# Optimization experiments

Measured on AMD Instinct MI355X. Metric: run time of the kernel, lower is better.

Reference implementation:

```python
import jax, jax.numpy as jnp
import numpy as np

D, E, H, K = 1024, 8, 4096, 2
B, S = 4, 2048


def setup_inputs() -> dict:
    key = jax.random.key(0)
    ks = jax.random.split(key, 5)
    scale = 0.02
    return {
        "x": jax.random.normal(ks[0], (B, S, D), dtype=jnp.float32),
        "gate_w": jax.random.normal(ks[1], (D, E), dtype=jnp.float32) * scale,
        "w1": jax.random.normal(ks[2], (E, D, H), dtype=jnp.float32) * scale,
        "b1": jnp.zeros((E, H), dtype=jnp.float32),
        "w2": jax.random.normal(ks[3], (E, H, D), dtype=jnp.float32) * scale,
        "b2": jnp.zeros((E, D), dtype=jnp.float32),
        "top_k": K,
    }


def reference(x, gate_w, w1, b1, w2, b2, top_k):
    orig_shape = x.shape
    d = x.shape[-1]
    xt = x.reshape(-1, d)                      # [T, D]
    T = xt.shape[0]

    # Gating: top-k over expert scores, softmax over the selected k.
    scores = xt @ gate_w                       # [T, E]
    expert_weights, expert_indices = jax.lax.top_k(scores, top_k)  # [T, K]
    expert_weights = jax.nn.softmax(expert_weights, axis=-1)

    # Dense all-expert MLP (GPT-style fc -> GELU -> proj), batched over experts.
    h = jnp.einsum('td,edh->eth', xt, w1) + b1[:, None, :]   # [E, T, H]
    h = jax.nn.gelu(h, approximate=False)
    outs = jnp.einsum('eth,ehd->etd', h, w2) + b2[:, None, :]  # [E, T, D]

    # Combine: gather each token's selected experts and mix with gate weights.
    tok = jnp.arange(T)[:, None]               # [T, 1]
    gathered = outs[expert_indices, tok]       # [T, K, D]
    y = jnp.sum(gathered * expert_weights[..., None], axis=1)  # [T, D]
    return y.reshape(orig_shape)
```

## Files before the change

### kernel.cpp

```cpp
#include <hip/hip_runtime.h>
#include <stdint.h>

#define T_TOK 8192
#define D_DIM 1024
#define E_NUM 8
#define H_DIM 4096

#define BM 128
#define BN 128
#define BK 64
#define NSEG 8
#define MAX_ROWS2 17408
#define MAX_MT2 (MAX_ROWS2/BM)

typedef unsigned short u16;
typedef __attribute__((ext_vector_type(8))) short shortx8;
typedef __attribute__((ext_vector_type(4))) float floatx4;
typedef __attribute__((ext_vector_type(8))) unsigned short ushortx8;

typedef const __attribute__((address_space(1))) unsigned int g_uint;
typedef __attribute__((address_space(3))) unsigned int l_uint;

__device__ __forceinline__ u16 f2bf(float f) {
  union { float f; unsigned int u; } v; v.f = f;
  unsigned int r = v.u + 0x7FFFu + ((v.u >> 16) & 1u);
  return (u16)(r >> 16);
}
__device__ __forceinline__ void gld_lds16(const u16* g, u16* l) {
  __builtin_amdgcn_global_load_lds((g_uint*)g, (l_uint*)l, 16, 0, 0);
}
__device__ __forceinline__ float gelu_fast(float v) {
  float y = v * (1.5957691216f + 0.07135481627f * v * v);
  y = fminf(y, 30.f);
  float ey = __expf(y);
  return v * ey * __builtin_amdgcn_rcpf(1.f + ey);
}

__global__ __launch_bounds__(256) void init_kernel(int* counts, int* fills, int* row_token) {
  int i = blockIdx.x * 256 + threadIdx.x;
  if (i < MAX_ROWS2) row_token[i] = -1;
  if (blockIdx.x == 0 && threadIdx.x < NSEG) { counts[threadIdx.x] = 0; fills[threadIdx.x] = 0; }
}

__global__ __launch_bounds__(256) void zero4_kernel(float4* out) {
  out[(size_t)blockIdx.x * 256 + threadIdx.x] = float4{0.f, 0.f, 0.f, 0.f};
}

__global__ __launch_bounds__(256) void convert_x_kernel(const float* __restrict__ X, u16* __restrict__ XC) {
  size_t i = ((size_t)blockIdx.x * 256 + threadIdx.x) * 8;
  float4 a = *(const float4*)&X[i];
  float4 b = *(const float4*)&X[i + 4];
  ushortx8 o;
  o[0] = f2bf(a.x); o[1] = f2bf(a.y); o[2] = f2bf(a.z); o[3] = f2bf(a.w);
  o[4] = f2bf(b.x); o[5] = f2bf(b.y); o[6] = f2bf(b.z); o[7] = f2bf(b.w);
  *(ushortx8*)&XC[i] = o;
}

__global__ __launch_bounds__(256) void gate_kernel(const float* __restrict__ X, const float* __restrict__ GW,
                                                   int* __restrict__ tk_idx, float* __restrict__ tk_w,
                                                   int* __restrict__ counts) {
  const int lane = threadIdx.x & 63;
  const int t = blockIdx.x * 4 + (threadIdx.x >> 6);
  const float4* xr4 = (const float4*)(X + (size_t)t * D_DIM + lane * 16);
  const float4* gw4 = (const float4*)GW;
  float acc[E_NUM];
#pragma unroll
  for (int e = 0; e < E_NUM; e++) acc[e] = 0.f;
#pragma unroll
  for (int i4 = 0; i4 < 4; i4++) {
    float4 xv = xr4[i4];
#pragma unroll
    for (int c = 0; c < 4; c++) {
      float xs = (&xv.x)[c];
      int d = lane * 16 + i4 * 4 + c;
      float4 g0 = gw4[d * 2], g1 = gw4[d * 2 + 1];
      acc[0] += xs * g0.x; acc[1] += xs * g0.y; acc[2] += xs * g0.z; acc[3] += xs * g0.w;
      acc[4] += xs * g1.x; acc[5] += xs * g1.y; acc[6] += xs * g1.z; acc[7] += xs * g1.w;
    }
  }
#pragma unroll
  for (int e = 0; e < E_NUM; e++)
    for (int off = 32; off; off >>= 1) acc[e] += __shfl_xor(acc[e], off);
  if (lane == 0) {
    int i0 = 0; float v0 = acc[0];
#pragma unroll
    for (int e = 1; e < E_NUM; e++) if (acc[e] > v0) { v0 = acc[e]; i0 = e; }
    int i1 = -1; float v1 = -1e30f;
#pragma unroll
    for (int e = 0; e < E_NUM; e++) if (e != i0 && acc[e] > v1) { v1 = acc[e]; i1 = e; }
    float e1 = expf(v1 - v0);
    float inv = 1.f / (1.f + e1);
    tk_idx[t * 2] = i0; tk_idx[t * 2 + 1] = i1;
    tk_w[t * 2] = inv;  tk_w[t * 2 + 1] = e1 * inv;
    atomicAdd(&counts[i0], 1); atomicAdd(&counts[i1], 1);
  }
}

__global__ void prefix_kernel(const int* counts, int* seg) {
  if (threadIdx.x == 0 && blockIdx.x == 0) {
    int a = 0;
    for (int i = 0; i < NSEG; i++) { seg[i] = a; a += ((counts[i] + BM - 1) / BM) * BM; }
    seg[NSEG] = a;
  }
}

__global__ __launch_bounds__(256) void fill_kernel(const int* __restrict__ tk_idx, const float* __restrict__ tk_w,
                                                   const int* __restrict__ seg, int* __restrict__ fills,
                                                   int* __restrict__ row_token, float* __restrict__ row_weight,
                                                   int* __restrict__ row_of) {
  int t = blockIdx.x * 256 + threadIdx.x;
  if (t >= T_TOK) return;
#pragma unroll
  for (int s = 0; s < 2; s++) {
    int sidx = tk_idx[t * 2 + s];
    int pos = atomicAdd(&fills[sidx], 1);
    int r = seg[sidx] + pos;
    row_token[r] = t; row_weight[r] = tk_w[t * 2 + s];
    row_of[t * 2 + s] = r;
  }
}

__global__ __launch_bounds__(256) void transpose_kernel(const float* __restrict__ src, u16* __restrict__ dst,
                                                        int R, int C) {
  __shared__ u16 tile[64][68];
  const int tid = threadIdx.x;
  size_t off = (size_t)blockIdx.z * (size_t)R * C;
  int r0 = blockIdx.y * 64, c0 = blockIdx.x * 64;
  int rr = tid >> 4, cc = (tid & 15) * 4;
#pragma unroll
  for (int i = 0; i < 4; i++) {
    int r = rr + i * 16;
    float4 v = *(const float4*)&src[off + (size_t)(r0 + r) * C + c0 + cc];
    u16* tp = &tile[r][cc];
    tp[0] = f2bf(v.x); tp[1] = f2bf(v.y); tp[2] = f2bf(v.z); tp[3] = f2bf(v.w);
  }
  __syncthreads();
  int c = tid >> 3, rb = (tid & 7) * 8;
#pragma unroll
  for (int i = 0; i < 2; i++) {
    int cx = c + i * 32;
    ushortx8 o;
#pragma unroll
    for (int q = 0; q < 8; q++) o[q] = tile[rb + q][cx];
    *(ushortx8*)&dst[off + (size_t)(c0 + cx) * R + r0 + rb] = o;
  }
}

__global__ __launch_bounds__(256, 3) void fc1_kernel(const u16* __restrict__ XC, const u16* __restrict__ W1T,
                                                     const float* __restrict__ B1, u16* __restrict__ Hbuf,
                                                     const int* __restrict__ row_token, const int* __restrict__ seg,
                                                     int mtile0, int e_filter) {
  const int mtile = mtile0 + blockIdx.y, ntile = blockIdx.x;
  const int row0 = mtile * BM;
  if (row0 >= seg[NSEG]) return;
  int sidx = 0;
#pragma unroll
  for (int i = 1; i < NSEG; i++) if (row0 >= seg[i]) sidx = i;
  const int e = sidx;
  if (e_filter >= 0 && e != e_filter) return;
  const size_t ebase = (e_filter >= 0) ? 0 : (size_t)e * H_DIM;
  const u16* Bbase = W1T + (ebase + (size_t)ntile * BN) * D_DIM;

  __shared__ u16 lA[BM * BK];
  __shared__ u16 lB[BN * BK];
  const int tid = threadIdx.x;
  const u16* gA[4]; const u16* gB[4];
#pragma unroll
  for (int r = 0; r < 4; r++) {
    int c = r * 256 + tid;
    int arow = c >> 3, acol = (c & 7) * 8;
    int tok = row_token[row0 + arow]; if (tok < 0) tok = 0;
    gA[r] = XC + (size_t)tok * D_DIM + acol;
    gB[r] = Bbase + (size_t)arow * D_DIM + acol;
  }
  const int lane = tid & 63;
  const int mq = (tid >> 7) & 1, nq = (tid >> 6) & 1;
  const int lrow = lane & 15, quad = lane >> 4;
  floatx4 acc[4][4];
#pragma unroll
  for (int i = 0; i < 4; i++)
#pragma unroll
    for (int j = 0; j < 4; j++)
#pragma unroll
      for (int r = 0; r < 4; r++) acc[i][j][r] = 0.f;

  for (int k0 = 0; k0 < D_DIM; k0 += BK) {
#pragma unroll
    for (int r = 0; r < 4; r++) gld_lds16(gA[r] + k0, &lA[(r * 256 + tid) * 8]);
#pragma unroll
    for (int r = 0; r < 4; r++) gld_lds16(gB[r] + k0, &lB[(r * 256 + tid) * 8]);
    __syncthreads();
#pragma unroll
    for (int kk = 0; kk < 2; kk++) {
      shortx8 af[4], bfr[4];
#pragma unroll
      for (int i = 0; i < 4; i++) af[i]  = *(const shortx8*)&lA[(mq * 64 + i * 16 + lrow) * BK + kk * 32 + quad * 8];
#pragma unroll
      for (int i = 0; i < 4; i++) bfr[i] = *(const shortx8*)&lB[(nq * 64 + i * 16 + lrow) * BK + kk * 32 + quad * 8];
#pragma unroll
      for (int i = 0; i < 4; i++)
#pragma unroll
        for (int j = 0; j < 4; j++)
          acc[i][j] = __builtin_amdgcn_mfma_f32_16x16x32_bf16(af[i], bfr[j], acc[i][j], 0, 0, 0);
    }
    __syncthreads();
  }
#pragma unroll
  for (int j = 0; j < 4; j++) {
    float bv = B1[(size_t)e * H_DIM + ntile * BN + nq * 64 + j * 16 + lrow];
#pragma unroll
    for (int i = 0; i < 4; i++)
#pragma unroll
      for (int rr = 0; rr < 4; rr++) {
        int hrow = (mtile - mtile0) * BM + mq * 64 + i * 16 + quad * 4 + rr;
        float v = acc[i][j][rr] + bv;
        Hbuf[(size_t)hrow * H_DIM + (size_t)ntile * BN + nq * 64 + j * 16 + lrow] = f2bf(gelu_fast(v));
      }
  }
}

__global__ __launch_bounds__(256, 3) void fc2_kernel(const u16* __restrict__ Hbuf, const u16* __restrict__ W2T,
                                                     const float* __restrict__ B2, float* __restrict__ outbuf,
                                                     const int* __restrict__ row_token, const float* __restrict__ row_weight,
                                                     const int* __restrict__ seg,
                                                     int mtile0, int e_filter) {
  const int mtile = mtile0 + blockIdx.y, ntile = blockIdx.x;
  const int row0 = mtile * BM;
  if (row0 >= seg[NSEG]) return;
  int sidx = 0;
#pragma unroll
  for (int i = 1; i < NSEG; i++) if (row0 >= seg[i]) sidx = i;
  const int e = sidx;
  if (e_filter >= 0 && e != e_filter) return;
  const size_t ebase = (e_filter >= 0) ? 0 : (size_t)e * D_DIM;
  const u16* Bbase = W2T + (ebase + (size_t)ntile * BN) * H_DIM;

  __shared__ u16 lA[BM * BK];
  __shared__ u16 lB[BN * BK];
  const int tid = threadIdx.x;
  const u16* gA[4]; const u16* gB[4];
#pragma unroll
  for (int r = 0; r < 4; r++) {
    int c = r * 256 + tid;
    int arow = c >> 3, acol = (c & 7) * 8;
    gA[r] = Hbuf + (size_t)((mtile - mtile0) * BM + arow) * H_DIM + acol;
    gB[r] = Bbase + (size_t)arow * H_DIM + acol;
  }
  const int lane = tid & 63;
  const int mq = (tid >> 7) & 1, nq = (tid >> 6) & 1;
  const int lrow = lane & 15, quad = lane >> 4;
  floatx4 acc[4][4];
#pragma unroll
  for (int i = 0; i < 4; i++)
#pragma unroll
    for (int j = 0; j < 4; j++)
#pragma unroll
      for (int r = 0; r < 4; r++) acc[i][j][r] = 0.f;

  for (int k0 = 0; k0 < H_DIM; k0 += BK) {
#pragma unroll
    for (int r = 0; r < 4; r++) gld_lds16(gA[r] + k0, &lA[(r * 256 + tid) * 8]);
#pragma unroll
    for (int r = 0; r < 4; r++) gld_lds16(gB[r] + k0, &lB[(r * 256 + tid) * 8]);
    __syncthreads();
#pragma unroll
    for (int kk = 0; kk < 2; kk++) {
      shortx8 af[4], bfr[4];
#pragma unroll
      for (int i = 0; i < 4; i++) af[i]  = *(const shortx8*)&lA[(mq * 64 + i * 16 + lrow) * BK + kk * 32 + quad * 8];
#pragma unroll
      for (int i = 0; i < 4; i++) bfr[i] = *(const shortx8*)&lB[(nq * 64 + i * 16 + lrow) * BK + kk * 32 + quad * 8];
#pragma unroll
      for (int i = 0; i < 4; i++)
#pragma unroll
        for (int j = 0; j < 4; j++)
          acc[i][j] = __builtin_amdgcn_mfma_f32_16x16x32_bf16(af[i], bfr[j], acc[i][j], 0, 0, 0);
    }
    __syncthreads();
  }
#pragma unroll
  for (int i = 0; i < 4; i++)
#pragma unroll
    for (int rr = 0; rr < 4; rr++) {
      int gr = row0 + mq * 64 + i * 16 + quad * 4 + rr;
      int tok = row_token[gr];
      if (tok >= 0) {
        float wgt = row_weight[gr];
        float* obase = outbuf + (size_t)gr * D_DIM + (size_t)ntile * BN + nq * 64 + lrow;
#pragma unroll
        for (int j = 0; j < 4; j++) {
          float bv = B2[(size_t)e * D_DIM + ntile * BN + nq * 64 + j * 16 + lrow];
          obase[j * 16] = (acc[i][j][rr] + bv) * wgt;
        }
      }
    }
}

__global__ __launch_bounds__(256) void combine_kernel(const float* __restrict__ outbuf, const int* __restrict__ row_of,
                                                      float* __restrict__ out) {
  int t = blockIdx.x;
  int d = threadIdx.x * 4;
  int r0 = row_of[t * 2], r1 = row_of[t * 2 + 1];
  float4 a = *(const float4*)&outbuf[(size_t)r0 * D_DIM + d];
  float4 b = *(const float4*)&outbuf[(size_t)r1 * D_DIM + d];
  *(float4*)&out[(size_t)t * D_DIM + d] = float4{a.x + b.x, a.y + b.y, a.z + b.z, a.w + b.w};
}

extern "C" void kernel_launch(void* const* d_in, const int* in_sizes, int n_in,
                              void* d_out, int out_size, void* d_ws, size_t ws_size,
                              hipStream_t stream) {
  const float* x  = (const float*)d_in[0];
  const float* gw = (const float*)d_in[1];
  const float* w1 = (const float*)d_in[2];
  const float* b1 = (const float*)d_in[3];
  const float* w2 = (const float*)d_in[4];
  const float* b2 = (const float*)d_in[5];
  float* out = (float*)d_out;

  char* p = (char*)d_ws;
  auto alloc = [&](size_t n) { char* q = p; p += (n + 255) & ~(size_t)255; return q; };
  int*   counts     = (int*)alloc(NSEG * 4);
  int*   fills      = (int*)alloc(NSEG * 4);
  int*   seg        = (int*)alloc((NSEG + 1) * 4);
  int*   tk_idx     = (int*)alloc((size_t)T_TOK * 2 * 4);
  float* tk_w       = (float*)alloc((size_t)T_TOK * 2 * 4);
  int*   row_token  = (int*)alloc((size_t)MAX_ROWS2 * 4);
  float* row_weight = (float*)alloc((size_t)MAX_ROWS2 * 4);
  int*   row_of     = (int*)alloc((size_t)T_TOK * 2 * 4);
  u16*   xc         = (u16*)alloc((size_t)T_TOK * D_DIM * 2);
  float* outbuf     = (float*)alloc((size_t)MAX_ROWS2 * D_DIM * 4);
  size_t meta = (size_t)(p - (char*)d_ws);

  const size_t Wfull = (size_t)E_NUM * H_DIM * D_DIM * 2;
  const size_t Wone  = (size_t)H_DIM * D_DIM * 2;
  auto hbytes = [](int n) { int cmx = (MAX_MT2 + n - 1) / n; return (size_t)cmx * BM * H_DIM * 2; };

  int mode = 3, N = 1;
  {
    const int cand[6] = {1, 2, 4, 8, 16, 32};
    for (int ci = 0; ci < 6 && mode == 3; ci++)
      if (meta + 2 * Wfull + hbytes(cand[ci]) <= ws_size) { mode = 0; N = cand[ci]; }
    for (int ci = 0; ci < 6 && mode == 3; ci++)
      if (meta + Wfull + hbytes(cand[ci]) <= ws_size) { mode = 1; N = cand[ci]; }
    for (int ci = 0; ci < 6 && mode == 3; ci++)
      if (meta + Wone + hbytes(cand[ci]) <= ws_size) { mode = 2; N = cand[ci]; }
  }

  if (mode == 3) {
    zero4_kernel<<<(int)(((size_t)T_TOK * D_DIM) / 1024), 256, 0, stream>>>((float4*)out);
    return;
  }

  u16 *W1T, *W2T;
  if (mode == 0) { W1T = (u16*)alloc(Wfull); W2T = (u16*)alloc(Wfull); }
  else           { W1T = W2T = (u16*)alloc(mode == 1 ? Wfull : Wone); }
  u16* Hbuf = (u16*)alloc(hbytes(N));
  const int cm = (MAX_MT2 + N - 1) / N;

  init_kernel<<<(MAX_ROWS2 + 255) / 256, 256, 0, stream>>>(counts, fills, row_token);
  convert_x_kernel<<<(int)(((size_t)T_TOK * D_DIM) / 2048), 256, 0, stream>>>(x, xc);
  gate_kernel<<<T_TOK / 4, 256, 0, stream>>>(x, gw, tk_idx, tk_w, counts);
  prefix_kernel<<<1, 64, 0, stream>>>(counts, seg);
  fill_kernel<<<T_TOK / 256, 256, 0, stream>>>(tk_idx, tk_w, seg, fills, row_token, row_weight, row_of);

  if (mode == 0) {
    transpose_kernel<<<dim3(H_DIM / 64, D_DIM / 64, E_NUM), 256, 0, stream>>>(w1, W1T, D_DIM, H_DIM);
    transpose_kernel<<<dim3(D_DIM / 64, H_DIM / 64, E_NUM), 256, 0, stream>>>(w2, W2T, H_DIM, D_DIM);
  }

  for (int c = 0; c < N; ++c) {
    int mtile0 = c * cm;
    int cmc = MAX_MT2 - mtile0; if (cmc > cm) cmc = cm; if (cmc <= 0) break;
    if (mode == 0) {
      fc1_kernel<<<dim3(H_DIM / BN, cmc), 256, 0, stream>>>(xc, W1T, b1, Hbuf, row_token, seg, mtile0, -1);
      fc2_kernel<<<dim3(D_DIM / BN, cmc), 256, 0, stream>>>(Hbuf, W2T, b2, outbuf, row_token, row_weight, seg, mtile0, -1);
    } else if (mode == 1) {
      transpose_kernel<<<dim3(H_DIM / 64, D_DIM / 64, E_NUM), 256, 0, stream>>>(w1, W1T, D_DIM, H_DIM);
      fc1_kernel<<<dim3(H_DIM / BN, cmc), 256, 0, stream>>>(xc, W1T, b1, Hbuf, row_token, seg, mtile0, -1);
      transpose_kernel<<<dim3(D_DIM / 64, H_DIM / 64, E_NUM), 256, 0, stream>>>(w2, W2T, H_DIM, D_DIM);
      fc2_kernel<<<dim3(D_DIM / BN, cmc), 256, 0, stream>>>(Hbuf, W2T, b2, outbuf, row_token, row_weight, seg, mtile0, -1);
    } else {
      for (int e = 0; e < E_NUM; e++) {
        transpose_kernel<<<dim3(H_DIM / 64, D_DIM / 64, 1), 256, 0, stream>>>(w1 + (size_t)e * D_DIM * H_DIM, W1T, D_DIM, H_DIM);
        fc1_kernel<<<dim3(H_DIM / BN, cmc), 256, 0, stream>>>(xc, W1T, b1, Hbuf, row_token, seg, mtile0, e);
      }
      for (int e = 0; e < E_NUM; e++) {
        transpose_kernel<<<dim3(D_DIM / 64, H_DIM / 64, 1), 256, 0, stream>>>(w2 + (size_t)e * H_DIM * D_DIM, W2T, H_DIM, D_DIM);
        fc2_kernel<<<dim3(D_DIM / BN, cmc), 256, 0, stream>>>(Hbuf, W2T, b2, outbuf, row_token, row_weight, seg, mtile0, e);
      }
    }
  }
  combine_kernel<<<T_TOK, 256, 0, stream>>>(outbuf, row_of, out);
}
```

Baseline: 1.025 ms.

## Fuse bf16 conversion into gating, remap blocks per XCD, stage fc1 output through LDS

Folds the fp32-to-bf16 conversion of x into the gate kernel so one kernel launch and one extra read of x are gone. The GEMM grids become 1D, and a decode step groups blocks so that consecutive m-tiles land on the same XCD, aiming for better L2 reuse of the weight tiles. The fc1 epilogue now writes its GELU output into a padded LDS tile and then stores it to global memory in coalesced 16-byte chunks. Global addresses are kept as 32-bit offsets, and launch bounds go from 3 to 4 waves, which adds register pressure and risks spills.

```diff
diff --git a/kernel.cpp b/kernel.cpp
--- a/kernel.cpp
+++ b/kernel.cpp
@@ -12,6 +12,7 @@
 #define NSEG 8
 #define MAX_ROWS2 17408
 #define MAX_MT2 (MAX_ROWS2/BM)
+#define LCS 136
 
 typedef unsigned short u16;
 typedef __attribute__((ext_vector_type(8))) short shortx8;
@@ -36,6 +37,17 @@
   return v * ey * __builtin_amdgcn_rcpf(1.f + ey);
 }
 
+__device__ __forceinline__ void decode_block(int flat, int NT, int cmc, int& ntile, int& mloc) {
+  if ((cmc & 7) == 0) {
+    int xcd = flat & 7, seq = flat >> 3;
+    ntile = seq & (NT - 1);
+    mloc = (seq / NT) * 8 + xcd;
+  } else {
+    ntile = flat & (NT - 1);
+    mloc = flat / NT;
+  }
+}
+
 __global__ __launch_bounds__(256) void init_kernel(int* counts, int* fills, int* row_token) {
   int i = blockIdx.x * 256 + threadIdx.x;
   if (i < MAX_ROWS2) row_token[i] = -1;
@@ -46,17 +58,8 @@
   out[(size_t)blockIdx.x * 256 + threadIdx.x] = float4{0.f, 0.f, 0.f, 0.f};
 }
 
-__global__ __launch_bounds__(256) void convert_x_kernel(const float* __restrict__ X, u16* __restrict__ XC) {
-  size_t i = ((size_t)blockIdx.x * 256 + threadIdx.x) * 8;
-  float4 a = *(const float4*)&X[i];
-  float4 b = *(const float4*)&X[i + 4];
-  ushortx8 o;
-  o[0] = f2bf(a.x); o[1] = f2bf(a.y); o[2] = f2bf(a.z); o[3] = f2bf(a.w);
-  o[4] = f2bf(b.x); o[5] = f2bf(b.y); o[6] = f2bf(b.z); o[7] = f2bf(b.w);
-  *(ushortx8*)&XC[i] = o;
-}
-
 __global__ __launch_bounds__(256) void gate_kernel(const float* __restrict__ X, const float* __restrict__ GW,
+                                                   u16* __restrict__ XC,
                                                    int* __restrict__ tk_idx, float* __restrict__ tk_w,
                                                    int* __restrict__ counts) {
   const int lane = threadIdx.x & 63;
@@ -66,18 +69,24 @@
   float acc[E_NUM];
 #pragma unroll
   for (int e = 0; e < E_NUM; e++) acc[e] = 0.f;
+  ushortx8 o0, o1;
 #pragma unroll
   for (int i4 = 0; i4 < 4; i4++) {
     float4 xv = xr4[i4];
 #pragma unroll
     for (int c = 0; c < 4; c++) {
       float xs = (&xv.x)[c];
-      int d = lane * 16 + i4 * 4 + c;
+      int q = i4 * 4 + c;
+      if (q < 8) o0[q] = f2bf(xs); else o1[q - 8] = f2bf(xs);
+      int d = lane * 16 + q;
       float4 g0 = gw4[d * 2], g1 = gw4[d * 2 + 1];
       acc[0] += xs * g0.x; acc[1] += xs * g0.y; acc[2] += xs * g0.z; acc[3] += xs * g0.w;
       acc[4] += xs * g1.x; acc[5] += xs * g1.y; acc[6] += xs * g1.z; acc[7] += xs * g1.w;
     }
   }
+  u16* xcb = XC + (size_t)t * D_DIM + lane * 16;
+  *(ushortx8*)xcb = o0;
+  *(ushortx8*)(xcb + 8) = o1;
 #pragma unroll
   for (int e = 0; e < E_NUM; e++)
     for (int off = 32; off; off >>= 1) acc[e] += __shfl_xor(acc[e], off);
@@ -146,11 +155,13 @@
   }
 }
 
-__global__ __launch_bounds__(256, 3) void fc1_kernel(const u16* __restrict__ XC, const u16* __restrict__ W1T,
+__global__ __launch_bounds__(256, 4) void fc1_kernel(const u16* __restrict__ XC, const u16* __restrict__ W1T,
                                                      const float* __restrict__ B1, u16* __restrict__ Hbuf,
                                                      const int* __restrict__ row_token, const int* __restrict__ seg,
-                                                     int mtile0, int e_filter) {
-  const int mtile = mtile0 + blockIdx.y, ntile = blockIdx.x;
+                                                     int mtile0, int cmc, int e_filter) {
+  int ntile, mloc;
+  decode_block(blockIdx.x, H_DIM / BN, cmc, ntile, mloc);
+  const int mtile = mtile0 + mloc;
   const int row0 = mtile * BM;
   if (row0 >= seg[NSEG]) return;
   int sidx = 0;
@@ -161,17 +172,18 @@
   const size_t ebase = (e_filter >= 0) ? 0 : (size_t)e * H_DIM;
   const u16* Bbase = W1T + (ebase + (size_t)ntile * BN) * D_DIM;
 
-  __shared__ u16 lA[BM * BK];
-  __shared__ u16 lB[BN * BK];
+  __shared__ u16 lds_u16[BM * LCS];
+  u16* lA = lds_u16;
+  u16* lB = lds_u16 + BM * BK;
   const int tid = threadIdx.x;
-  const u16* gA[4]; const u16* gB[4];
+  const int sub = tid >> 3, acol = (tid & 7) * 8;
+  unsigned int offA[4], offB[4];
 #pragma unroll
   for (int r = 0; r < 4; r++) {
-    int c = r * 256 + tid;
-    int arow = c >> 3, acol = (c & 7) * 8;
+    int arow = r * 32 + sub;
     int tok = row_token[row0 + arow]; if (tok < 0) tok = 0;
-    gA[r] = XC + (size_t)tok * D_DIM + acol;
-    gB[r] = Bbase + (size_t)arow * D_DIM + acol;
+    offA[r] = (unsigned int)tok * D_DIM + acol;
+    offB[r] = (unsigned int)arow * D_DIM + acol;
   }
   const int lane = tid & 63;
   const int mq = (tid >> 7) & 1, nq = (tid >> 6) & 1;
@@ -186,9 +198,9 @@
 
   for (int k0 = 0; k0 < D_DIM; k0 += BK) {
 #pragma unroll
-    for (int r = 0; r < 4; r++) gld_lds16(gA[r] + k0, &lA[(r * 256 + tid) * 8]);
-#pragma unroll
-    for (int r = 0; r < 4; r++) gld_lds16(gB[r] + k0, &lB[(r * 256 + tid) * 8]);
+    for (int r = 0; r < 4; r++) gld_lds16(XC + offA[r] + k0, &lA[(r * 256 + tid) * 8]);
+#pragma unroll
+    for (int r = 0; r < 4; r++) gld_lds16(Bbase + offB[r] + k0, &lB[(r * 256 + tid) * 8]);
     __syncthreads();
 #pragma unroll
     for (int kk = 0; kk < 2; kk++) {
@@ -208,23 +220,35 @@
 #pragma unroll
   for (int j = 0; j < 4; j++) {
     float bv = B1[(size_t)e * H_DIM + ntile * BN + nq * 64 + j * 16 + lrow];
-#pragma unroll
-    for (int i = 0; i < 4; i++)
+    int col = nq * 64 + j * 16 + lrow;
+#pragma unroll
+    for (int i = 0; i < 4; i++) {
+      int row = mq * 64 + i * 16 + quad * 4;
 #pragma unroll
       for (int rr = 0; rr < 4; rr++) {
-        int hrow = (mtile - mtile0) * BM + mq * 64 + i * 16 + quad * 4 + rr;
         float v = acc[i][j][rr] + bv;
-        Hbuf[(size_t)hrow * H_DIM + (size_t)ntile * BN + nq * 64 + j * 16 + lrow] = f2bf(gelu_fast(v));
+        lds_u16[(row + rr) * LCS + col] = f2bf(gelu_fast(v));
       }
-  }
-}
-
-__global__ __launch_bounds__(256, 3) void fc2_kernel(const u16* __restrict__ Hbuf, const u16* __restrict__ W2T,
+    }
+  }
+  __syncthreads();
+  {
+    const int r = tid >> 1, c0 = (tid & 1) * 64;
+    size_t gbase = (size_t)(mloc * BM + r) * H_DIM + (size_t)ntile * BN + c0;
+#pragma unroll
+    for (int q = 0; q < 8; q++)
+      *(ushortx8*)&Hbuf[gbase + q * 8] = *(const ushortx8*)&lds_u16[r * LCS + c0 + q * 8];
+  }
+}
+
+__global__ __launch_bounds__(256, 4) void fc2_kernel(const u16* __restrict__ Hbuf, const u16* __restrict__ W2T,
                                                      const float* __restrict__ B2, float* __restrict__ outbuf,
                                                      const int* __restrict__ row_token, const float* __restrict__ row_weight,
                                                      const int* __restrict__ seg,
-                                                     int mtile0, int e_filter) {
-  const int mtile = mtile0 + blockIdx.y, ntile = blockIdx.x;
+                                                     int mtile0, int cmc, int e_filter) {
+  int ntile, mloc;
+  decode_block(blockIdx.x, D_DIM / BN, cmc, ntile, mloc);
+  const int mtile = mtile0 + mloc;
   const int row0 = mtile * BM;
   if (row0 >= seg[NSEG]) return;
   int sidx = 0;
@@ -238,13 +262,13 @@
   __shared__ u16 lA[BM * BK];
   __shared__ u16 lB[BN * BK];
   const int tid = threadIdx.x;
-  const u16* gA[4]; const u16* gB[4];
+  const int sub = tid >> 3, acol = (tid & 7) * 8;
+  unsigned int offA[4], offB[4];
 #pragma unroll
   for (int r = 0; r < 4; r++) {
-    int c = r * 256 + tid;
-    int arow = c >> 3, acol = (c & 7) * 8;
-    gA[r] = Hbuf + (size_t)((mtile - mtile0) * BM + arow) * H_DIM + acol;
-    gB[r] = Bbase + (size_t)arow * H_DIM + acol;
+    int arow = r * 32 + sub;
+    offA[r] = (unsigned int)(mloc * BM + arow) * H_DIM + acol;
+    offB[r] = (unsigned int)arow * H_DIM + acol;
   }
   const int lane = tid & 63;
   const int mq = (tid >> 7) & 1, nq = (tid >> 6) & 1;
@@ -259,9 +283,9 @@
 
   for (int k0 = 0; k0 < H_DIM; k0 += BK) {
 #pragma unroll
-    for (int r = 0; r < 4; r++) gld_lds16(gA[r] + k0, &lA[(r * 256 + tid) * 8]);
-#pragma unroll
-    for (int r = 0; r < 4; r++) gld_lds16(gB[r] + k0, &lB[(r * 256 + tid) * 8]);
+    for (int r = 0; r < 4; r++) gld_lds16(Hbuf + offA[r] + k0, &lA[(r * 256 + tid) * 8]);
+#pragma unroll
+    for (int r = 0; r < 4; r++) gld_lds16(Bbase + offB[r] + k0, &lB[(r * 256 + tid) * 8]);
     __syncthreads();
 #pragma unroll
     for (int kk = 0; kk < 2; kk++) {
@@ -358,8 +382,7 @@
   const int cm = (MAX_MT2 + N - 1) / N;
 
   init_kernel<<<(MAX_ROWS2 + 255) / 256, 256, 0, stream>>>(counts, fills, row_token);
-  convert_x_kernel<<<(int)(((size_t)T_TOK * D_DIM) / 2048), 256, 0, stream>>>(x, xc);
-  gate_kernel<<<T_TOK / 4, 256, 0, stream>>>(x, gw, tk_idx, tk_w, counts);
+  gate_kernel<<<T_TOK / 4, 256, 0, stream>>>(x, gw, xc, tk_idx, tk_w, counts);
   prefix_kernel<<<1, 64, 0, stream>>>(counts, seg);
   fill_kernel<<<T_TOK / 256, 256, 0, stream>>>(tk_idx, tk_w, seg, fills, row_token, row_weight, row_of);
 
@@ -372,21 +395,21 @@
     int mtile0 = c * cm;
     int cmc = MAX_MT2 - mtile0; if (cmc > cm) cmc = cm; if (cmc <= 0) break;
     if (mode == 0) {
-      fc1_kernel<<<dim3(H_DIM / BN, cmc), 256, 0, stream>>>(xc, W1T, b1, Hbuf, row_token, seg, mtile0, -1);
-      fc2_kernel<<<dim3(D_DIM / BN, cmc), 256, 0, stream>>>(Hbuf, W2T, b2, outbuf, row_token, row_weight, seg, mtile0, -1);
+      fc1_kernel<<<cmc * (H_DIM / BN), 256, 0, stream>>>(xc, W1T, b1, Hbuf, row_token, seg, mtile0, cmc, -1);
+      fc2_kernel<<<cmc * (D_DIM / BN), 256, 0, stream>>>(Hbuf, W2T, b2, outbuf, row_token, row_weight, seg, mtile0, cmc, -1);
     } else if (mode == 1) {
       transpose_kernel<<<dim3(H_DIM / 64, D_DIM / 64, E_NUM), 256, 0, stream>>>(w1, W1T, D_DIM, H_DIM);
-      fc1_kernel<<<dim3(H_DIM / BN, cmc), 256, 0, stream>>>(xc, W1T, b1, Hbuf, row_token, seg, mtile0, -1);
+      fc1_kernel<<<cmc * (H_DIM / BN), 256, 0, stream>>>(xc, W1T, b1, Hbuf, row_token, seg, mtile0, cmc, -1);
       transpose_kernel<<<dim3(D_DIM / 64, H_DIM / 64, E_NUM), 256, 0, stream>>>(w2, W2T, H_DIM, D_DIM);
-      fc2_kernel<<<dim3(D_DIM / BN, cmc), 256, 0, stream>>>(Hbuf, W2T, b2, outbuf, row_token, row_weight, seg, mtile0, -1);
+      fc2_kernel<<<cmc * (D_DIM / BN), 256, 0, stream>>>(Hbuf, W2T, b2, outbuf, row_token, row_weight, seg, mtile0, cmc, -1);
     } else {
       for (int e = 0; e < E_NUM; e++) {
         transpose_kernel<<<dim3(H_DIM / 64, D_DIM / 64, 1), 256, 0, stream>>>(w1 + (size_t)e * D_DIM * H_DIM, W1T, D_DIM, H_DIM);
-        fc1_kernel<<<dim3(H_DIM / BN, cmc), 256, 0, stream>>>(xc, W1T, b1, Hbuf, row_token, seg, mtile0, e);
+        fc1_kernel<<<cmc * (H_DIM / BN), 256, 0, stream>>>(xc, W1T, b1, Hbuf, row_token, seg, mtile0, cmc, e);
       }
       for (int e = 0; e < E_NUM; e++) {
         transpose_kernel<<<dim3(D_DIM / 64, H_DIM / 64, 1), 256, 0, stream>>>(w2 + (size_t)e * H_DIM * D_DIM, W2T, H_DIM, D_DIM);
-        fc2_kernel<<<dim3(D_DIM / BN, cmc), 256, 0, stream>>>(Hbuf, W2T, b2, outbuf, row_token, row_weight, seg, mtile0, e);
+        fc2_kernel<<<cmc * (D_DIM / BN), 256, 0, stream>>>(Hbuf, W2T, b2, outbuf, row_token, row_weight, seg, mtile0, cmc, e);
       }
     }
   }
```

After: 1.030 ms. No clear change (+0.4%).
